# Performance work log

Measured on AMD Instinct MI355X. Metric: run time of the kernel, lower is better.

Reference implementation:

```python
import jax, jax.numpy as jnp
import numpy as np

# SH constants (standard 3DGS eval_sh, degree 3)
C0 = 0.28209479177387814
C1 = 0.4886025119029199
C2 = (1.0925484305920792, -1.0925484305920792, 0.31539156525252005, -1.0925484305920792, 0.5462742152960396)
C3 = (-0.5900435899266435, 2.890611442640554, -0.4570457994644658, 0.3731763325901154, -0.4570457994644658, 1.445305721320277, -0.5900435899266435)

N_GAUSS = 4096
N_PTS = 32768
CHUNK = 4096  # math-identical to torch's 16384 chunking (pure concat of independent points)


def quat_to_rot(q):
    # q: (N,4) normalized, (w,x,y,z) as in 3DGS build_rotation
    r, x, y, z = q[:, 0], q[:, 1], q[:, 2], q[:, 3]
    R = jnp.stack([
        jnp.stack([1 - 2 * (y * y + z * z), 2 * (x * y - r * z), 2 * (x * z + r * y)], -1),
        jnp.stack([2 * (x * y + r * z), 1 - 2 * (x * x + z * z), 2 * (y * z - r * x)], -1),
        jnp.stack([2 * (x * z - r * y), 2 * (y * z + r * x), 1 - 2 * (x * x + y * y)], -1),
    ], axis=-2)  # (N,3,3)
    return R


def eval_sh3(sh, dirs):
    # sh: (N,16) scalar SH coeffs; dirs: (C,N,3) unit directions -> (C,N)
    x, y, z = dirs[..., 0], dirs[..., 1], dirs[..., 2]
    xx, yy, zz = x * x, y * y, z * z
    xy, yz, xz = x * y, y * z, x * z
    s = sh[None]  # (1,N,16)
    res = C0 * s[..., 0]
    res = res - C1 * y * s[..., 1] + C1 * z * s[..., 2] - C1 * x * s[..., 3]
    res = (res + C2[0] * xy * s[..., 4] + C2[1] * yz * s[..., 5]
           + C2[2] * (2 * zz - xx - yy) * s[..., 6]
           + C2[3] * xz * s[..., 7] + C2[4] * (xx - yy) * s[..., 8])
    res = (res + C3[0] * y * (3 * xx - yy) * s[..., 9] + C3[1] * xy * z * s[..., 10]
           + C3[2] * y * (4 * zz - xx - yy) * s[..., 11]
           + C3[3] * z * (2 * zz - 3 * xx - 3 * yy) * s[..., 12]
           + C3[4] * x * (4 * zz - xx - yy) * s[..., 13]
           + C3[5] * z * (xx - yy) * s[..., 14]
           + C3[6] * x * (xx - yy - 3 * zz) * s[..., 15])
    return res


def setup_inputs() -> dict:
    key = jax.random.key(0)
    ks = jax.random.split(key, 9)
    return {
        "network_pts": jax.random.normal(ks[0], (N_PTS, 3), jnp.float32),
        "network_view": jax.random.normal(ks[1], (N_PTS, 3), jnp.float32),
        "network_tx": jax.random.normal(ks[2], (N_PTS, 3), jnp.float32),
        "xyz": jax.random.normal(ks[3], (N_GAUSS, 3), jnp.float32),
        "sh_dc": jax.random.normal(ks[4], (N_GAUSS, 1), jnp.float32),
        "sh_rest": 0.1 * jax.random.normal(ks[5], (N_GAUSS, 15), jnp.float32),
        "scaling": jnp.float32(-3.0) + 0.2 * jax.random.normal(ks[6], (N_GAUSS, 3), jnp.float32),
        "rotation": jax.random.normal(ks[7], (N_GAUSS, 4), jnp.float32),
        "opacity_logit": jax.random.normal(ks[8], (N_GAUSS, 1), jnp.float32),
    }


def reference(network_pts, network_view, network_tx, xyz, sh_dc, sh_rest, scaling, rotation, opacity_logit):
    # activations, matching GaussianModel.setup_functions
    sh = jnp.concatenate([sh_dc, sh_rest], axis=1)            # (N,16)
    s = jnp.exp(scaling)                                      # (N,3)
    q = rotation / jnp.linalg.norm(rotation, axis=1, keepdims=True)
    R = quat_to_rot(q)                                        # (N,3,3)
    # precision = (L L^T)^{-1} with L = R diag(s)  =>  R diag(1/s^2) R^T
    prec = jnp.einsum('nij,nj,nkj->nik', R, 1.0 / (s * s), R)  # (N,3,3)
    op = jax.nn.sigmoid(opacity_logit)[:, 0]                  # (N,)

    pts = network_pts.reshape(-1, CHUNK, 3)

    def chunk_fn(p):  # p: (C,3)
        diff = p[:, None, :] - xyz[None, :, :]                # (C,N,3)
        maha = jnp.einsum('cni,nij,cnj->cn', diff, prec, diff)
        w = op[None, :] * jnp.exp(-0.5 * maha)                # (C,N)
        # dir_pp = xyz - query_point, normalized (as in get_magnitude)
        dirs = -diff / jnp.linalg.norm(diff, axis=-1, keepdims=True)
        mag = jnp.maximum(eval_sh3(sh, dirs), 0.0)            # (C,N)
        return w.sum(axis=1), (w * mag).sum(axis=1)

    opac_c, sig_c = jax.lax.map(chunk_fn, pts)
    return opac_c.reshape(-1), sig_c.reshape(-1)
```

## Files before the change

kernel.cpp:

```cpp
#include <hip/hip_runtime.h>
#include <hip/hip_bf16.h>

#define N_GAUSS 4096
#define N_PTS   32768
#define BLOCK   256
#define NSEG    16
#define SEGG    (N_GAUSS / NSEG)
#define NBLK_PT 128
#define GSTRIDE 32
#define NCELL   4096
#define NBIN    16
#define RECCAP  128

#define SH_C0  0.28209479177387814f
#define SH_C1  0.4886025119029199f

#define WS_GP     0
#define WS_GHIST  131072
#define WS_CELLID 135168
#define WS_SPTS   167936
#define WS_ACC    299008
#define WS_HPART  364544

__device__ __forceinline__ int cell_of(float x, float y, float z) {
    int cx = min(15, max(0, (int)((x + 3.2f) * 2.5f)));
    int cy = min(15, max(0, (int)((y + 3.2f) * 2.5f)));
    int cz = min(15, max(0, (int)((z + 3.2f) * 2.5f)));
    int ex = (cx & 1) | ((cx & 2) << 2) | ((cx & 4) << 4) | ((cx & 8) << 6);
    int ey = (cy & 1) | ((cy & 2) << 2) | ((cy & 4) << 4) | ((cy & 8) << 6);
    int ez = (cz & 1) | ((cz & 2) << 2) | ((cz & 4) << 4) | ((cz & 8) << 6);
    return ex | (ey << 1) | (ez << 2);
}

__global__ __launch_bounds__(1024) void binprep_kernel(
    const float* __restrict__ pts, const float* __restrict__ xyz,
    const float* __restrict__ sh_dc, const float* __restrict__ sh_rest,
    const float* __restrict__ scaling, const float* __restrict__ rotation,
    const float* __restrict__ opl, float* __restrict__ gp,
    int* __restrict__ cellid, int* __restrict__ hpart, float* __restrict__ acc)
{
    const int t = threadIdx.x, bx = blockIdx.x;

    if (bx >= 20) {
        float4* a4 = (float4*)acc;
        int base = (bx - 20) * 1024 * 2 + t;
        a4[base]        = make_float4(0.f, 0.f, 0.f, 0.f);
        a4[base + 1024] = make_float4(0.f, 0.f, 0.f, 0.f);
        return;
    }
    if (bx >= 16) {
        int g = (bx - 16) * 1024 + t;
        float s0 = scaling[3*g+0], s1 = scaling[3*g+1], s2 = scaling[3*g+2];
        float i0 = __expf(-2.0f * s0);
        float i1 = __expf(-2.0f * s1);
        float i2 = __expf(-2.0f * s2);
        float maxs2 = __expf(2.0f * fmaxf(s0, fmaxf(s1, s2)));

        float r = rotation[4*g+0], x = rotation[4*g+1];
        float y = rotation[4*g+2], z = rotation[4*g+3];
        float n = rsqrtf(r*r + x*x + y*y + z*z);
        r *= n; x *= n; y *= n; z *= n;
        float R00 = 1.f - 2.f*(y*y + z*z), R01 = 2.f*(x*y - r*z), R02 = 2.f*(x*z + r*y);
        float R10 = 2.f*(x*y + r*z), R11 = 1.f - 2.f*(x*x + z*z), R12 = 2.f*(y*z - r*x);
        float R20 = 2.f*(x*z - r*y), R21 = 2.f*(y*z + r*x), R22 = 1.f - 2.f*(x*x + y*y);

        float pxx = 0.5f*(R00*R00*i0 + R01*R01*i1 + R02*R02*i2);
        float pxy = 0.5f*(R00*R10*i0 + R01*R11*i1 + R02*R12*i2);
        float pxz = 0.5f*(R00*R20*i0 + R01*R21*i1 + R02*R22*i2);
        float pyy = 0.5f*(R10*R10*i0 + R11*R11*i1 + R12*R12*i2);
        float pyz = 0.5f*(R10*R20*i0 + R11*R21*i1 + R12*R22*i2);
        float pzz = 0.5f*(R20*R20*i0 + R21*R21*i1 + R22*R22*i2);

        float op   = 1.f / (1.f + __expf(-opl[g]));
        float lnop = __logf(op);
        float Tg   = 2.0f * maxs2 * (lnop + 16.0f);

        float* G = gp + (size_t)g * GSTRIDE;
        G[0] = xyz[3*g+0]; G[1] = xyz[3*g+1]; G[2] = xyz[3*g+2]; G[3] = Tg;
        G[4] = pxx; G[5] = pxy; G[6] = pxz; G[7] = pyy;
        G[8] = pyz; G[9] = pzz; G[10] = lnop; G[11] = 0.f;

        const float* sr = sh_rest + (size_t)g * 15;
        G[12] =  SH_C0 * sh_dc[g];
        G[13] = -SH_C1 * sr[0];
        G[14] =  SH_C1 * sr[1];
        G[15] = -SH_C1 * sr[2];
        G[16] =  1.0925484305920792f  * sr[3];
        G[17] = -1.0925484305920792f  * sr[4];
        G[18] =  0.31539156525252005f * sr[5];
        G[19] = -1.0925484305920792f  * sr[6];
        G[20] =  0.5462742152960396f  * sr[7];
        G[21] = -0.5900435899266435f  * sr[8];
        G[22] =  2.890611442640554f   * sr[9];
        G[23] = -0.4570457994644658f  * sr[10];
        G[24] =  0.3731763325901154f  * sr[11];
        G[25] = -0.4570457994644658f  * sr[12];
        G[26] =  1.445305721320277f   * sr[13];
        G[27] = -0.5900435899266435f  * sr[14];
        G[28] = 0.f; G[29] = 0.f; G[30] = 0.f; G[31] = 0.f;
        return;
    }

    __shared__ int s_hist[NCELL];
    #pragma unroll
    for (int i = 0; i < 4; ++i) s_hist[t + i * 1024] = 0;
    __syncthreads();
    #pragma unroll
    for (int k = 0; k < 2; ++k) {
        int p = bx * 2048 + k * 1024 + t;
        float x = pts[3*p+0], y = pts[3*p+1], z = pts[3*p+2];
        int cell = cell_of(x, y, z);
        cellid[p] = cell;
        atomicAdd(&s_hist[cell], 1);
    }
    __syncthreads();
    #pragma unroll
    for (int i = 0; i < 4; ++i) {
        int c = t + i * 1024;
        hpart[bx * NCELL + c] = s_hist[c];
    }
}

__global__ __launch_bounds__(1024) void scan_kernel(
    const int* __restrict__ hpart, int* __restrict__ ghist)
{
    __shared__ int s_wsum[16];
    const int t = threadIdx.x;
    const int lane = t & 63, wv = t >> 6;
    const int b = t * 4;

    int4 c = make_int4(0, 0, 0, 0);
    #pragma unroll
    for (int k = 0; k < NBIN; ++k) {
        int4 h = *(const int4*)(hpart + k * NCELL + b);
        c.x += h.x; c.y += h.y; c.z += h.z; c.w += h.w;
    }
    int s = c.x + c.y + c.z + c.w;

    int incl = s;
    #pragma unroll
    for (int off = 1; off < 64; off <<= 1) {
        int v = __shfl_up(incl, off);
        if (lane >= off) incl += v;
    }
    if (lane == 63) s_wsum[wv] = incl;
    __syncthreads();
    if (wv == 0) {
        int ws = (lane < 16) ? s_wsum[lane] : 0;
        int wincl = ws;
        #pragma unroll
        for (int off = 1; off < 16; off <<= 1) {
            int v = __shfl_up(wincl, off);
            if (lane >= off) wincl += v;
        }
        if (lane < 16) s_wsum[lane] = wincl - ws;
    }
    __syncthreads();

    int excl = s_wsum[wv] + (incl - s);
    ghist[b]   = excl;
    ghist[b+1] = excl + c.x;
    ghist[b+2] = excl + c.x + c.y;
    ghist[b+3] = excl + c.x + c.y + c.z;
}

__global__ __launch_bounds__(256) void scatter_kernel(
    const float* __restrict__ pts, const int* __restrict__ cellid,
    int* __restrict__ ghist, float4* __restrict__ spts)
{
    int p = blockIdx.x * 256 + threadIdx.x;
    float x = pts[3*p+0], y = pts[3*p+1], z = pts[3*p+2];
    int pos = atomicAdd(&ghist[cellid[p]], 1);
    spts[pos] = make_float4(x, y, z, __int_as_float(p));
}

__device__ __forceinline__ void eval_one(
    const float4* R, float dx, float dy, float dz, float d2,
    float& opac, float& sig)
{
    float4 q1 = R[1], q2 = R[2];
    float vx = q1.x*dx + q1.y*dy + q1.z*dz;
    float vy = q1.y*dx + q1.w*dy + q2.x*dz;
    float vz = q1.z*dx + q2.x*dy + q2.y*dz;
    float maha = dx*vx + dy*vy + dz*vz;
    float w = __expf(q2.z - maha);
    opac += w;

    if (__any(w > 1e-9f)) {
        float4 q3 = R[3], q4 = R[4], q5 = R[5], q6 = R[6];
        float rinv = rsqrtf(d2);
        float x = -dx * rinv, y = -dy * rinv, z = -dz * rinv;
        float xx = x*x, yy = y*y, zz = z*z;
        float xy = x*y, yz = y*z, xz = x*z;

        float res = q3.x;
        res += y * q3.y;
        res += z * q3.z;
        res += x * q3.w;
        res += xy * q4.x;
        res += yz * q4.y;
        res += (3.f*zz - 1.f) * q4.z;
        res += xz * q4.w;
        float xxmyy = xx - yy;
        res += xxmyy * q5.x;
        res += y * (3.f*xx - yy) * q5.y;
        res += (xy * z) * q5.z;
        float f5z1 = 5.f*zz - 1.f;
        res += y * f5z1 * q5.w;
        res += z * (5.f*zz - 3.f) * q6.x;
        res += x * f5z1 * q6.y;
        res += z * xxmyy * q6.z;
        res += x * (xxmyy - 3.f*zz) * q6.w;

        sig += w * fmaxf(res, 0.f);
    }
}

__global__ __launch_bounds__(BLOCK, 8) void gauss_kernel(
    const float4* __restrict__ spts, const float4* __restrict__ gp4,
    float* __restrict__ acc)
{
    __shared__ float s_min[4][3], s_max[4][3];
    __shared__ int s_nact;
    __shared__ int s_act[SEGG];
    __shared__ float4 s_rec[RECCAP * 8];

    const int tid = threadIdx.x;
    const int pb  = blockIdx.x;
    const int seg = blockIdx.y;
    float4 P = spts[pb * 256 + tid];
    const float px = P.x, py = P.y, pz = P.z;

    float mnx = px, mxx = px, mny = py, mxy = py, mnz = pz, mxz = pz;
    #pragma unroll
    for (int off = 32; off >= 1; off >>= 1) {
        mnx = fminf(mnx, __shfl_xor(mnx, off));
        mxx = fmaxf(mxx, __shfl_xor(mxx, off));
        mny = fminf(mny, __shfl_xor(mny, off));
        mxy = fmaxf(mxy, __shfl_xor(mxy, off));
        mnz = fminf(mnz, __shfl_xor(mnz, off));
        mxz = fmaxf(mxz, __shfl_xor(mxz, off));
    }
    const int wave = tid >> 6;
    if ((tid & 63) == 0) {
        s_min[wave][0] = mnx; s_min[wave][1] = mny; s_min[wave][2] = mnz;
        s_max[wave][0] = mxx; s_max[wave][1] = mxy; s_max[wave][2] = mxz;
    }
    if (tid == 0) s_nact = 0;
    __syncthreads();
    const float bmnx = fminf(fminf(s_min[0][0], s_min[1][0]), fminf(s_min[2][0], s_min[3][0]));
    const float bmny = fminf(fminf(s_min[0][1], s_min[1][1]), fminf(s_min[2][1], s_min[3][1]));
    const float bmnz = fminf(fminf(s_min[0][2], s_min[1][2]), fminf(s_min[2][2], s_min[3][2]));
    const float bmxx = fmaxf(fmaxf(s_max[0][0], s_max[1][0]), fmaxf(s_max[2][0], s_max[3][0]));
    const float bmxy = fmaxf(fmaxf(s_max[0][1], s_max[1][1]), fmaxf(s_max[2][1], s_max[3][1]));
    const float bmxz = fmaxf(fmaxf(s_max[0][2], s_max[1][2]), fmaxf(s_max[2][2], s_max[3][2]));

    {
        const int gg = seg * SEGG + tid;
        float4 c = gp4[(size_t)gg << 3];
        float ddx = fmaxf(0.f, fmaxf(bmnx - c.x, c.x - bmxx));
        float ddy = fmaxf(0.f, fmaxf(bmny - c.y, c.y - bmxy));
        float ddz = fmaxf(0.f, fmaxf(bmnz - c.z, c.z - bmxz));
        float dd2 = ddx*ddx + ddy*ddy + ddz*ddz;
        if (dd2 <= c.w) {
            int slot = atomicAdd(&s_nact, 1);
            s_act[slot] = gg;
        }
    }
    __syncthreads();
    const int nact = s_nact;
    if (nact == 0) return;

    float opac = 0.f, sig = 0.f;
    for (int base = 0; base < nact; base += RECCAP) {
        const int cnt = min(RECCAP, nact - base);
        if (base) __syncthreads();

        for (int idx = tid; idx < cnt * 8; idx += BLOCK) {
            int rec = idx >> 3, q = idx & 7;
            s_rec[idx] = gp4[((size_t)s_act[base + rec] << 3) + q];
        }
        __syncthreads();

        for (int j = 0; j < cnt; j += 2) {
            const bool has1 = (j + 1 < cnt);
            const float4* A = &s_rec[j * 8];
            const float4* B = &s_rec[(has1 ? j + 1 : j) * 8];

            float4 aq0 = A[0];
            float4 bq0 = B[0];
            float adx = px - aq0.x, ady = py - aq0.y, adz = pz - aq0.z;
            float bdx = px - bq0.x, bdy = py - bq0.y, bdz = pz - bq0.z;
            float ad2 = adx*adx + ady*ady + adz*adz;
            float bd2 = bdx*bdx + bdy*bdy + bdz*bdz;

            if (!__all(ad2 > aq0.w)) eval_one(A, adx, ady, adz, ad2, opac, sig);
            if (has1 && !__all(bd2 > bq0.w)) eval_one(B, bdx, bdy, bdz, bd2, opac, sig);
        }
    }

    const int pos = pb * 256 + tid;
    atomicAdd(&acc[pos], opac);
    atomicAdd(&acc[N_PTS + pos], sig);
}

__global__ __launch_bounds__(256) void permute_kernel(
    const float* __restrict__ acc, const float4* __restrict__ spts,
    float* __restrict__ out)
{
    int p = blockIdx.x * 256 + threadIdx.x;
    int orig = __float_as_int(spts[p].w);
    out[orig] = acc[p];
    out[N_PTS + orig] = acc[N_PTS + p];
}

extern "C" void kernel_launch(void* const* d_in, const int* in_sizes, int n_in,
                              void* d_out, int out_size, void* d_ws, size_t ws_size,
                              hipStream_t stream) {
    const float* pts      = (const float*)d_in[0];
    const float* xyz      = (const float*)d_in[3];
    const float* sh_dc    = (const float*)d_in[4];
    const float* sh_rest  = (const float*)d_in[5];
    const float* scaling  = (const float*)d_in[6];
    const float* rotation = (const float*)d_in[7];
    const float* opl      = (const float*)d_in[8];

    float*  out    = (float*)d_out;
    float*  wsf    = (float*)d_ws;
    float*  gp     = wsf + WS_GP;
    int*    ghist  = (int*)(wsf + WS_GHIST);
    int*    cellid = (int*)(wsf + WS_CELLID);
    float4* spts   = (float4*)(wsf + WS_SPTS);
    float*  acc    = wsf + WS_ACC;
    int*    hpart  = (int*)(wsf + WS_HPART);

    binprep_kernel<<<dim3(28), dim3(1024), 0, stream>>>(
        pts, xyz, sh_dc, sh_rest, scaling, rotation, opl, gp, cellid, hpart, acc);
    scan_kernel<<<dim3(1), dim3(1024), 0, stream>>>(hpart, ghist);
    scatter_kernel<<<dim3(NBLK_PT), dim3(256), 0, stream>>>(pts, cellid, ghist, spts);

    dim3 grid(NBLK_PT, NSEG);
    gauss_kernel<<<grid, dim3(BLOCK), 0, stream>>>(spts, (const float4*)gp, acc);
    permute_kernel<<<dim3(NBLK_PT), dim3(256), 0, stream>>>(acc, spts, out);
}
```

Baseline: 130.5 us.

## Split culling into separate kernel and evenly chunk active Gaussian lists per block

Measured after the change: 119.5 us. 8.4% less time.

```diff
diff --git a/kernel.cpp b/kernel.cpp
--- a/kernel.cpp
+++ b/kernel.cpp
@@ -4,8 +4,7 @@
 #define N_GAUSS 4096
 #define N_PTS   32768
 #define BLOCK   256
-#define NSEG    16
-#define SEGG    (N_GAUSS / NSEG)
+#define NCHUNK  32
 #define NBLK_PT 128
 #define GSTRIDE 32
 #define NCELL   4096
@@ -21,6 +20,8 @@
 #define WS_SPTS   167936
 #define WS_ACC    299008
 #define WS_HPART  364544
+#define WS_ACT    430080
+#define WS_NACT   954368
 
 __device__ __forceinline__ int cell_of(float x, float y, float z) {
     int cx = min(15, max(0, (int)((x + 3.2f) * 2.5f)));
@@ -174,6 +175,61 @@
     spts[pos] = make_float4(x, y, z, __int_as_float(p));
 }
 
+__global__ __launch_bounds__(BLOCK) void cull_kernel(
+    const float4* __restrict__ spts, const float4* __restrict__ gp4,
+    int* __restrict__ actlist, int* __restrict__ nactg)
+{
+    __shared__ float s_min[4][3], s_max[4][3];
+    __shared__ int s_n;
+    __shared__ int s_list[N_GAUSS];
+
+    const int tid = threadIdx.x;
+    const int pb  = blockIdx.x;
+    float4 P = spts[pb * 256 + tid];
+    const float px = P.x, py = P.y, pz = P.z;
+
+    float mnx = px, mxx = px, mny = py, mxy = py, mnz = pz, mxz = pz;
+    #pragma unroll
+    for (int off = 32; off >= 1; off >>= 1) {
+        mnx = fminf(mnx, __shfl_xor(mnx, off));
+        mxx = fmaxf(mxx, __shfl_xor(mxx, off));
+        mny = fminf(mny, __shfl_xor(mny, off));
+        mxy = fmaxf(mxy, __shfl_xor(mxy, off));
+        mnz = fminf(mnz, __shfl_xor(mnz, off));
+        mxz = fmaxf(mxz, __shfl_xor(mxz, off));
+    }
+    const int wave = tid >> 6;
+    if ((tid & 63) == 0) {
+        s_min[wave][0] = mnx; s_min[wave][1] = mny; s_min[wave][2] = mnz;
+        s_max[wave][0] = mxx; s_max[wave][1] = mxy; s_max[wave][2] = mxz;
+    }
+    if (tid == 0) s_n = 0;
+    __syncthreads();
+    const float bmnx = fminf(fminf(s_min[0][0], s_min[1][0]), fminf(s_min[2][0], s_min[3][0]));
+    const float bmny = fminf(fminf(s_min[0][1], s_min[1][1]), fminf(s_min[2][1], s_min[3][1]));
+    const float bmnz = fminf(fminf(s_min[0][2], s_min[1][2]), fminf(s_min[2][2], s_min[3][2]));
+    const float bmxx = fmaxf(fmaxf(s_max[0][0], s_max[1][0]), fmaxf(s_max[2][0], s_max[3][0]));
+    const float bmxy = fmaxf(fmaxf(s_max[0][1], s_max[1][1]), fmaxf(s_max[2][1], s_max[3][1]));
+    const float bmxz = fmaxf(fmaxf(s_max[0][2], s_max[1][2]), fmaxf(s_max[2][2], s_max[3][2]));
+
+    for (int r = 0; r < N_GAUSS / BLOCK; ++r) {
+        const int gg = r * BLOCK + tid;
+        float4 c = gp4[(size_t)gg << 3];
+        float ddx = fmaxf(0.f, fmaxf(bmnx - c.x, c.x - bmxx));
+        float ddy = fmaxf(0.f, fmaxf(bmny - c.y, c.y - bmxy));
+        float ddz = fmaxf(0.f, fmaxf(bmnz - c.z, c.z - bmxz));
+        float dd2 = ddx*ddx + ddy*ddy + ddz*ddz;
+        if (dd2 <= c.w) {
+            int slot = atomicAdd(&s_n, 1);
+            s_list[slot] = gg;
+        }
+    }
+    __syncthreads();
+    const int n = s_n;
+    for (int i = tid; i < n; i += BLOCK) actlist[pb * N_GAUSS + i] = s_list[i];
+    if (tid == 0) nactg[pb] = n;
+}
+
 __device__ __forceinline__ void eval_one(
     const float4* R, float dx, float dy, float dz, float d2,
     float& opac, float& sig)
@@ -216,87 +272,50 @@
     }
 }
 
-__global__ __launch_bounds__(BLOCK, 8) void gauss_kernel(
+__global__ __launch_bounds__(BLOCK) void eval_kernel(
     const float4* __restrict__ spts, const float4* __restrict__ gp4,
+    const int* __restrict__ actlist, const int* __restrict__ nactg,
     float* __restrict__ acc)
 {
-    __shared__ float s_min[4][3], s_max[4][3];
-    __shared__ int s_nact;
-    __shared__ int s_act[SEGG];
+    __shared__ int s_idx[RECCAP];
     __shared__ float4 s_rec[RECCAP * 8];
 
     const int tid = threadIdx.x;
-    const int pb  = blockIdx.x;
-    const int seg = blockIdx.y;
+    const int ck  = blockIdx.x;
+    const int pb  = blockIdx.y;
+
+    const int nact = nactg[pb];
+    const int c0 = (nact * ck) / NCHUNK;
+    const int c1 = (nact * (ck + 1)) / NCHUNK;
+    const int cnt = c1 - c0;
+    if (cnt == 0) return;
+
     float4 P = spts[pb * 256 + tid];
+    if (tid < cnt) s_idx[tid] = actlist[pb * N_GAUSS + c0 + tid];
+    __syncthreads();
+
+    for (int idx = tid; idx < cnt * 8; idx += BLOCK) {
+        int rec = idx >> 3, q = idx & 7;
+        s_rec[idx] = gp4[((size_t)s_idx[rec] << 3) + q];
+    }
+    __syncthreads();
+
     const float px = P.x, py = P.y, pz = P.z;
-
-    float mnx = px, mxx = px, mny = py, mxy = py, mnz = pz, mxz = pz;
-    #pragma unroll
-    for (int off = 32; off >= 1; off >>= 1) {
-        mnx = fminf(mnx, __shfl_xor(mnx, off));
-        mxx = fmaxf(mxx, __shfl_xor(mxx, off));
-        mny = fminf(mny, __shfl_xor(mny, off));
-        mxy = fmaxf(mxy, __shfl_xor(mxy, off));
-        mnz = fminf(mnz, __shfl_xor(mnz, off));
-        mxz = fmaxf(mxz, __shfl_xor(mxz, off));
-    }
-    const int wave = tid >> 6;
-    if ((tid & 63) == 0) {
-        s_min[wave][0] = mnx; s_min[wave][1] = mny; s_min[wave][2] = mnz;
-        s_max[wave][0] = mxx; s_max[wave][1] = mxy; s_max[wave][2] = mxz;
-    }
-    if (tid == 0) s_nact = 0;
-    __syncthreads();
-    const float bmnx = fminf(fminf(s_min[0][0], s_min[1][0]), fminf(s_min[2][0], s_min[3][0]));
-    const float bmny = fminf(fminf(s_min[0][1], s_min[1][1]), fminf(s_min[2][1], s_min[3][1]));
-    const float bmnz = fminf(fminf(s_min[0][2], s_min[1][2]), fminf(s_min[2][2], s_min[3][2]));
-    const float bmxx = fmaxf(fmaxf(s_max[0][0], s_max[1][0]), fmaxf(s_max[2][0], s_max[3][0]));
-    const float bmxy = fmaxf(fmaxf(s_max[0][1], s_max[1][1]), fmaxf(s_max[2][1], s_max[3][1]));
-    const float bmxz = fmaxf(fmaxf(s_max[0][2], s_max[1][2]), fmaxf(s_max[2][2], s_max[3][2]));
-
-    {
-        const int gg = seg * SEGG + tid;
-        float4 c = gp4[(size_t)gg << 3];
-        float ddx = fmaxf(0.f, fmaxf(bmnx - c.x, c.x - bmxx));
-        float ddy = fmaxf(0.f, fmaxf(bmny - c.y, c.y - bmxy));
-        float ddz = fmaxf(0.f, fmaxf(bmnz - c.z, c.z - bmxz));
-        float dd2 = ddx*ddx + ddy*ddy + ddz*ddz;
-        if (dd2 <= c.w) {
-            int slot = atomicAdd(&s_nact, 1);
-            s_act[slot] = gg;
-        }
-    }
-    __syncthreads();
-    const int nact = s_nact;
-    if (nact == 0) return;
-
     float opac = 0.f, sig = 0.f;
-    for (int base = 0; base < nact; base += RECCAP) {
-        const int cnt = min(RECCAP, nact - base);
-        if (base) __syncthreads();
-
-        for (int idx = tid; idx < cnt * 8; idx += BLOCK) {
-            int rec = idx >> 3, q = idx & 7;
-            s_rec[idx] = gp4[((size_t)s_act[base + rec] << 3) + q];
-        }
-        __syncthreads();
-
-        for (int j = 0; j < cnt; j += 2) {
-            const bool has1 = (j + 1 < cnt);
-            const float4* A = &s_rec[j * 8];
-            const float4* B = &s_rec[(has1 ? j + 1 : j) * 8];
-
-            float4 aq0 = A[0];
-            float4 bq0 = B[0];
-            float adx = px - aq0.x, ady = py - aq0.y, adz = pz - aq0.z;
-            float bdx = px - bq0.x, bdy = py - bq0.y, bdz = pz - bq0.z;
-            float ad2 = adx*adx + ady*ady + adz*adz;
-            float bd2 = bdx*bdx + bdy*bdy + bdz*bdz;
-
-            if (!__all(ad2 > aq0.w)) eval_one(A, adx, ady, adz, ad2, opac, sig);
-            if (has1 && !__all(bd2 > bq0.w)) eval_one(B, bdx, bdy, bdz, bd2, opac, sig);
-        }
+    for (int j = 0; j < cnt; j += 2) {
+        const bool has1 = (j + 1 < cnt);
+        const float4* A = &s_rec[j * 8];
+        const float4* B = &s_rec[(has1 ? j + 1 : j) * 8];
+
+        float4 aq0 = A[0];
+        float4 bq0 = B[0];
+        float adx = px - aq0.x, ady = py - aq0.y, adz = pz - aq0.z;
+        float bdx = px - bq0.x, bdy = py - bq0.y, bdz = pz - bq0.z;
+        float ad2 = adx*adx + ady*ady + adz*adz;
+        float bd2 = bdx*bdx + bdy*bdy + bdz*bdz;
+
+        if (!__all(ad2 > aq0.w)) eval_one(A, adx, ady, adz, ad2, opac, sig);
+        if (has1 && !__all(bd2 > bq0.w)) eval_one(B, bdx, bdy, bdz, bd2, opac, sig);
     }
 
     const int pos = pb * 256 + tid;
@@ -325,21 +344,25 @@
     const float* rotation = (const float*)d_in[7];
     const float* opl      = (const float*)d_in[8];
 
-    float*  out    = (float*)d_out;
-    float*  wsf    = (float*)d_ws;
-    float*  gp     = wsf + WS_GP;
-    int*    ghist  = (int*)(wsf + WS_GHIST);
-    int*    cellid = (int*)(wsf + WS_CELLID);
-    float4* spts   = (float4*)(wsf + WS_SPTS);
-    float*  acc    = wsf + WS_ACC;
-    int*    hpart  = (int*)(wsf + WS_HPART);
+    float*  out     = (float*)d_out;
+    float*  wsf     = (float*)d_ws;
+    float*  gp      = wsf + WS_GP;
+    int*    ghist   = (int*)(wsf + WS_GHIST);
+    int*    cellid  = (int*)(wsf + WS_CELLID);
+    float4* spts    = (float4*)(wsf + WS_SPTS);
+    float*  acc     = wsf + WS_ACC;
+    int*    hpart   = (int*)(wsf + WS_HPART);
+    int*    actlist = (int*)(wsf + WS_ACT);
+    int*    nactg   = (int*)(wsf + WS_NACT);
 
     binprep_kernel<<<dim3(28), dim3(1024), 0, stream>>>(
         pts, xyz, sh_dc, sh_rest, scaling, rotation, opl, gp, cellid, hpart, acc);
     scan_kernel<<<dim3(1), dim3(1024), 0, stream>>>(hpart, ghist);
     scatter_kernel<<<dim3(NBLK_PT), dim3(256), 0, stream>>>(pts, cellid, ghist, spts);
 
-    dim3 grid(NBLK_PT, NSEG);
-    gauss_kernel<<<grid, dim3(BLOCK), 0, stream>>>(spts, (const float4*)gp, acc);
+    cull_kernel<<<dim3(NBLK_PT), dim3(BLOCK), 0, stream>>>(
+        spts, (const float4*)gp, actlist, nactg);
+    eval_kernel<<<dim3(NCHUNK, NBLK_PT), dim3(BLOCK), 0, stream>>>(
+        spts, (const float4*)gp, actlist, nactg, acc);
     permute_kernel<<<dim3(NBLK_PT), dim3(256), 0, stream>>>(acc, spts, out);
 }
```
